# Kernel tuning notes

Measured on AMD Instinct MI355X. Metric: run time of the kernel, lower is better.

## Reference

```python
import jax, jax.numpy as jnp
import numpy as np

B, C, H, W = 4, 512, 128, 128   # batch, in_channels, feature map HxW
KC = 256                        # key_channels
KP = 150                        # number of proxy regions (ADE20K classes)


def conv1x1(x, w, b):
    # x: [b,c,h,w], w: [k,c], b: [k] -> [b,k,h,w]
    return jnp.einsum('bchw,kc->bkhw', x, w) + b[None, :, None, None]


def proj2(x, w1, b1, w2, b2):
    # conv1x1-(BN folded)-relu twice, as in f_pixel / f_object
    h = jax.nn.relu(conv1x1(x, w1, b1))
    return jax.nn.relu(conv1x1(h, w2, b2))


def setup_inputs() -> dict:
    key = jax.random.key(0)
    ks = jax.random.split(key, 16)
    nrm = lambda k, shape, s=0.05: (jax.random.normal(k, shape, jnp.float32) * s)
    return {
        'x': jax.random.normal(ks[0], (B, C, H, W), jnp.float32),
        'proxy_feats': jax.random.normal(ks[1], (B, C, KP, 1), jnp.float32),
        # f_pixel: two 1x1 convs (BN in eval mode folded into weight+bias)
        'w_p1': nrm(ks[2], (KC, C)), 'b_p1': nrm(ks[3], (KC,)),
        'w_p2': nrm(ks[4], (KC, KC)), 'b_p2': nrm(ks[5], (KC,)),
        # f_object
        'w_o1': nrm(ks[6], (KC, C)), 'b_o1': nrm(ks[7], (KC,)),
        'w_o2': nrm(ks[8], (KC, KC)), 'b_o2': nrm(ks[9], (KC,)),
        # f_down
        'w_d': nrm(ks[10], (KC, C)), 'b_d': nrm(ks[11], (KC,)),
        # f_up
        'w_u': nrm(ks[12], (C, KC)), 'b_u': nrm(ks[13], (C,)),
    }


def reference(x, proxy_feats, w_p1, b_p1, w_p2, b_p2, w_o1, b_o1, w_o2, b_o2,
              w_d, b_d, w_u, b_u):
    b, _, h, w = x.shape
    n = h * w
    # query: [b, n, kc]
    query = proj2(x, w_p1, b_p1, w_p2, b_p2).reshape(b, KC, n).transpose(0, 2, 1)
    # key: [b, kc, kp]
    k = proj2(proxy_feats, w_o1, b_o1, w_o2, b_o2).reshape(b, KC, KP)
    # value: [b, kp, kc]
    v = jax.nn.relu(conv1x1(proxy_feats, w_d, b_d)).reshape(b, KC, KP).transpose(0, 2, 1)
    # scaled dot-product cross-attention
    sim = jnp.einsum('bnc,bck->bnk', query, k) * (KC ** -0.5)
    sim = jax.nn.softmax(sim, axis=-1)
    context = jnp.einsum('bnk,bkc->bnc', sim, v)            # [b, n, kc]
    context = context.transpose(0, 2, 1).reshape(b, KC, h, w)
    return jax.nn.relu(conv1x1(context, w_u, b_u))           # [b, C, h, w]
```

## Files before the change

### kernel.cpp

```cpp
#include <hip/hip_runtime.h>
#include <hip/hip_bf16.h>

#define NB   4
#define CIN  512
#define NPX  16384
#define KC   256
#define KP   150

#define LDH  264
#define LDP  200
#define LDX  72
#define SHSZ 16896
#define XBOF 7680

typedef __attribute__((ext_vector_type(8))) short short8;
typedef __attribute__((ext_vector_type(4))) float f32x4;
typedef __attribute__((ext_vector_type(4))) unsigned int u32x4;
typedef unsigned short u16;

__device__ __forceinline__ u16 f2bf(float f) {
    unsigned int u = __float_as_uint(f);
    return (u16)((u + 0x7FFFu + ((u >> 16) & 1u)) >> 16);
}
__device__ __forceinline__ unsigned cvtpk(float lo, float hi) {
    unsigned r;
    asm("v_cvt_pk_bf16_f32 %0, %1, %2" : "=v"(r) : "v"(lo), "v"(hi));
    return r;
}
__device__ __forceinline__ short8 ldfrag(const u16* __restrict__ p, int idx) {
    return *(const short8*)(p + ((long)idx << 3));
}

__global__ __launch_bounds__(256, 4)
void fused_kernel(const u16* __restrict__ wp1p, const float* __restrict__ xg,
                  const u16* __restrict__ wp2p, const float* __restrict__ bp1,
                  const float* __restrict__ bp2, const u16* __restrict__ keyp,
                  const u16* __restrict__ vp, const u16* __restrict__ wup,
                  const float* __restrict__ bu, float* __restrict__ outg)
{
    __shared__ u16 sh[SHSZ];

    const int b  = blockIdx.z;
    const int n0 = blockIdx.x * 64;
    const int tid = threadIdx.x, lane = tid & 63, wid = tid >> 6;
    const int rg = lane & 15, kg = lane >> 4;

    const float* xb = xg + (long)b * CIN * NPX;
    float* ob       = outg + (long)b * CIN * NPX;
    const u16* kyp  = keyp + (long)b * 40960;
    const u16* vbp  = vp   + (long)b * 40960;

    const int sxp = (tid & 31) * 2, sxg = tid >> 5;
    const float* xsrc = xb + (long)(sxg * 8) * NPX + n0 + sxp;
    u16* XB = sh + XBOF;

    float f0[8], f1[8];
    auto LOADX = [&](int kt) {
        #pragma unroll
        for (int e = 0; e < 8; ++e) {
            float2 v = *(const float2*)(xsrc + (long)(kt * 64 + e) * NPX);
            f0[e] = v.x; f1[e] = v.y;
        }
    };
    auto WRITEX = [&](int buf) {
        u32x4 w0, w1;
        w0.x = cvtpk(f0[0], f0[1]); w0.y = cvtpk(f0[2], f0[3]);
        w0.z = cvtpk(f0[4], f0[5]); w0.w = cvtpk(f0[6], f0[7]);
        w1.x = cvtpk(f1[0], f1[1]); w1.y = cvtpk(f1[2], f1[3]);
        w1.z = cvtpk(f1[4], f1[5]); w1.w = cvtpk(f1[6], f1[7]);
        *(u32x4*)(XB + buf * 4608 + sxp * LDX + sxg * 8) = w0;
        *(u32x4*)(XB + buf * 4608 + (sxp + 1) * LDX + sxg * 8) = w1;
    };

    f32x4 acc[4][4];
    #pragma unroll
    for (int i = 0; i < 4; ++i)
        #pragma unroll
        for (int j = 0; j < 4; ++j) acc[i][j] = (f32x4){0.f, 0.f, 0.f, 0.f};

    LOADX(0); WRITEX(0);
    __syncthreads();

    #pragma unroll 1
    for (int kt = 0; kt < 8; ++kt) {
        const int buf = kt & 1;
        if (kt < 7) LOADX(kt + 1);
        #pragma unroll 1
        for (int s = 0; s < 2; ++s) {
            short8 a[4];
            #pragma unroll
            for (int i = 0; i < 4; ++i)
                a[i] = ldfrag(wp1p, ((wid * 4 + i) * 16 + kt * 2 + s) * 64 + lane);
            __builtin_amdgcn_s_setprio(1);
            #pragma unroll
            for (int j = 0; j < 4; ++j) {
                short8 bb = *(const short8*)(XB + buf * 4608 + (j * 16 + rg) * LDX + (s * 4 + kg) * 8);
                #pragma unroll
                for (int i = 0; i < 4; ++i)
                    acc[i][j] = __builtin_amdgcn_mfma_f32_16x16x32_bf16(a[i], bb, acc[i][j], 0, 0, 0);
            }
            __builtin_amdgcn_s_setprio(0);
        }
        if (kt < 7) WRITEX(buf ^ 1);
        __syncthreads();
    }

    #pragma unroll
    for (int i = 0; i < 4; ++i) {
        const int kc4 = wid * 64 + i * 16 + kg * 4;
        const f32x4 bv = *(const f32x4*)(bp1 + kc4);
        #pragma unroll
        for (int j = 0; j < 4; ++j) {
            const int n = j * 16 + rg;
            uint2 pk;
            pk.x = cvtpk(fmaxf(acc[i][j][0] + bv.x, 0.f), fmaxf(acc[i][j][1] + bv.y, 0.f));
            pk.y = cvtpk(fmaxf(acc[i][j][2] + bv.z, 0.f), fmaxf(acc[i][j][3] + bv.w, 0.f));
            *(uint2*)(sh + n * LDH + kc4) = pk;
        }
    }
    __syncthreads();

    f32x4 acc2[4][4];
    #pragma unroll
    for (int i = 0; i < 4; ++i)
        #pragma unroll
        for (int j = 0; j < 4; ++j) acc2[i][j] = (f32x4){0.f, 0.f, 0.f, 0.f};

    #pragma unroll 1
    for (int S = 0; S < 8; ++S) {
        short8 a[4];
        #pragma unroll
        for (int i = 0; i < 4; ++i)
            a[i] = ldfrag(wp2p, ((wid * 4 + i) * 8 + S) * 64 + lane);
        __builtin_amdgcn_s_setprio(1);
        #pragma unroll
        for (int j = 0; j < 4; ++j) {
            short8 bb = *(const short8*)(sh + (j * 16 + rg) * LDH + S * 32 + kg * 8);
            #pragma unroll
            for (int i = 0; i < 4; ++i)
                acc2[i][j] = __builtin_amdgcn_mfma_f32_16x16x32_bf16(a[i], bb, acc2[i][j], 0, 0, 0);
        }
        __builtin_amdgcn_s_setprio(0);
    }
    __syncthreads();

    #pragma unroll
    for (int i = 0; i < 4; ++i) {
        const int kc4 = wid * 64 + i * 16 + kg * 4;
        const f32x4 bv = *(const f32x4*)(bp2 + kc4);
        #pragma unroll
        for (int j = 0; j < 4; ++j) {
            const int n = j * 16 + rg;
            uint2 pk;
            pk.x = cvtpk(fmaxf(acc2[i][j][0] + bv.x, 0.f), fmaxf(acc2[i][j][1] + bv.y, 0.f));
            pk.y = cvtpk(fmaxf(acc2[i][j][2] + bv.z, 0.f), fmaxf(acc2[i][j][3] + bv.w, 0.f));
            *(uint2*)(sh + n * LDH + kc4) = pk;
        }
    }
    __syncthreads();

    f32x4 s1[10];
    #pragma unroll
    for (int i = 0; i < 10; ++i) s1[i] = (f32x4){0.f, 0.f, 0.f, 0.f};
    #pragma unroll 1
    for (int s = 0; s < 8; ++s) {
        short8 bq = *(const short8*)(sh + (wid * 16 + rg) * LDH + s * 32 + kg * 8);
        __builtin_amdgcn_s_setprio(1);
        #pragma unroll
        for (int i = 0; i < 10; ++i) {
            short8 a = ldfrag(kyp, (i * 8 + s) * 64 + lane);
            s1[i] = __builtin_amdgcn_mfma_f32_16x16x32_bf16(a, bq, s1[i], 0, 0, 0);
        }
        __builtin_amdgcn_s_setprio(0);
    }
    float mx = -3.0e38f;
    #pragma unroll
    for (int i = 0; i < 9; ++i)
        #pragma unroll
        for (int r = 0; r < 4; ++r) mx = fmaxf(mx, s1[i][r]);
    #pragma unroll
    for (int r = 0; r < 4; ++r) if (kg * 4 + r < 6) mx = fmaxf(mx, s1[9][r]);
    mx = fmaxf(mx, __shfl_xor(mx, 16));
    mx = fmaxf(mx, __shfl_xor(mx, 32));
    float l = 0.f;
    #pragma unroll
    for (int i = 0; i < 10; ++i)
        #pragma unroll
        for (int r = 0; r < 4; ++r) {
            const bool valid = (i < 9) || (kg * 4 + r < 6);
            float e = valid ? __expf((s1[i][r] - mx) * 0.0625f) : 0.f;
            s1[i][r] = e; l += e;
        }
    l += __shfl_xor(l, 16);
    l += __shfl_xor(l, 32);
    const float inv = 1.f / l;
    __syncthreads();

    #pragma unroll
    for (int i = 0; i < 10; ++i) {
        uint2 pk;
        pk.x = cvtpk(s1[i][0] * inv, s1[i][1] * inv);
        pk.y = cvtpk(s1[i][2] * inv, s1[i][3] * inv);
        *(uint2*)(sh + (wid * 16 + rg) * LDP + i * 16 + kg * 4) = pk;
    }
    __syncthreads();

    f32x4 acc4[4][4];
    #pragma unroll
    for (int i = 0; i < 4; ++i)
        #pragma unroll
        for (int j = 0; j < 4; ++j) acc4[i][j] = (f32x4){0.f, 0.f, 0.f, 0.f};
    #pragma unroll 1
    for (int s = 0; s < 5; ++s) {
        short8 a[4];
        #pragma unroll
        for (int i = 0; i < 4; ++i)
            a[i] = ldfrag(vbp, ((wid * 4 + i) * 5 + s) * 64 + lane);
        __builtin_amdgcn_s_setprio(1);
        #pragma unroll
        for (int j = 0; j < 4; ++j) {
            short8 bb = *(const short8*)(sh + (j * 16 + rg) * LDP + s * 32 + kg * 8);
            #pragma unroll
            for (int i = 0; i < 4; ++i)
                acc4[i][j] = __builtin_amdgcn_mfma_f32_16x16x32_bf16(a[i], bb, acc4[i][j], 0, 0, 0);
        }
        __builtin_amdgcn_s_setprio(0);
    }
    __syncthreads();

    #pragma unroll
    for (int i = 0; i < 4; ++i) {
        const int kc4 = wid * 64 + i * 16 + kg * 4;
        #pragma unroll
        for (int j = 0; j < 4; ++j) {
            const int n = j * 16 + rg;
            uint2 pk;
            pk.x = cvtpk(acc4[i][j][0], acc4[i][j][1]);
            pk.y = cvtpk(acc4[i][j][2], acc4[i][j][3]);
            *(uint2*)(sh + n * LDH + kc4) = pk;
        }
    }
    __syncthreads();

    #pragma unroll 1
    for (int h2 = 0; h2 < 2; ++h2) {
        f32x4 a5[4][4];
        #pragma unroll
        for (int i = 0; i < 4; ++i)
            #pragma unroll
            for (int j = 0; j < 4; ++j) a5[i][j] = (f32x4){0.f, 0.f, 0.f, 0.f};
        #pragma unroll 1
        for (int S = 0; S < 8; ++S) {
            short8 a[4];
            #pragma unroll
            for (int i = 0; i < 4; ++i)
                a[i] = ldfrag(wup, ((h2 * 16 + wid * 4 + i) * 8 + S) * 64 + lane);
            __builtin_amdgcn_s_setprio(1);
            #pragma unroll
            for (int j = 0; j < 4; ++j) {
                short8 bb = *(const short8*)(sh + (j * 16 + rg) * LDH + S * 32 + kg * 8);
                #pragma unroll
                for (int i = 0; i < 4; ++i)
                    a5[i][j] = __builtin_amdgcn_mfma_f32_16x16x32_bf16(a[i], bb, a5[i][j], 0, 0, 0);
            }
            __builtin_amdgcn_s_setprio(0);
        }
        #pragma unroll
        for (int i = 0; i < 4; ++i) {
            const int c4 = h2 * 256 + wid * 64 + i * 16 + kg * 4;
            const f32x4 bv = *(const f32x4*)(bu + c4);
            #pragma unroll
            for (int j = 0; j < 4; ++j) {
                const int n = n0 + j * 16 + rg;
                ob[(long)(c4 + 0) * NPX + n] = fmaxf(a5[i][j][0] + bv.x, 0.f);
                ob[(long)(c4 + 1) * NPX + n] = fmaxf(a5[i][j][1] + bv.y, 0.f);
                ob[(long)(c4 + 2) * NPX + n] = fmaxf(a5[i][j][2] + bv.z, 0.f);
                ob[(long)(c4 + 3) * NPX + n] = fmaxf(a5[i][j][3] + bv.w, 0.f);
            }
        }
    }
}

__global__ __launch_bounds__(256)
void prep_kernel(const float* __restrict__ w_p1, const float* __restrict__ w_p2,
                 const float* __restrict__ w_u,  const float* __restrict__ w_o1,
                 const float* __restrict__ w_o2, const float* __restrict__ w_d,
                 u16* __restrict__ wp1p, u16* __restrict__ wp2p,
                 u16* __restrict__ wup, float* __restrict__ wo1T,
                 float* __restrict__ wdT, float* __restrict__ wo2T)
{
    const int i = blockIdx.x * 256 + threadIdx.x;
    const int j = i & 7, l = (i >> 3) & 63;
    {
        const int S = (i >> 9) & 15, R = i >> 13;
        wp1p[i] = f2bf(w_p1[(long)(R * 16 + (l & 15)) * CIN + S * 32 + ((l >> 4) << 3) + j]);
    }
    {
        const int S = (i >> 9) & 7, R = i >> 12;
        wup[i] = f2bf(w_u[(long)(R * 16 + (l & 15)) * KC + S * 32 + ((l >> 4) << 3) + j]);
    }
    {
        const int c = i >> 8, kc = i & 255;
        wo1T[i] = w_o1[(long)kc * CIN + c];
        wdT[i]  = w_d [(long)kc * CIN + c];
    }
    if (i < 65536) {
        const int S = (i >> 9) & 7, R = i >> 12;
        wp2p[i] = f2bf(w_p2[(long)(R * 16 + (l & 15)) * KC + S * 32 + ((l >> 4) << 3) + j]);
        const int c = i >> 8, kc = i & 255;
        wo2T[i] = w_o2[(long)kc * KC + c];
    }
}

__global__ __launch_bounds__(256)
void kv_kernel(const float* __restrict__ proxy,
               const float* __restrict__ wo1T, const float* __restrict__ b_o1,
               const float* __restrict__ wdT,  const float* __restrict__ b_d,
               const float* __restrict__ wo2T, const float* __restrict__ b_o2,
               u16* __restrict__ keyp, u16* __restrict__ vp)
{
    __shared__ float PX[CIN * 4];
    __shared__ float HL[4][KC];
    const int kp0 = blockIdx.x * 4;
    const int b   = blockIdx.y;
    const int kc  = threadIdx.x;

    #pragma unroll
    for (int it = 0; it < 8; ++it) {
        const int idx = it * 256 + kc;
        const int q = idx & 3, c = idx >> 2;
        const int kp = kp0 + q;
        PX[c * 4 + q] = (kp < KP) ? proxy[(long)b * CIN * KP + (long)c * KP + kp] : 0.f;
    }
    __syncthreads();

    float ah[4] = {0.f, 0.f, 0.f, 0.f}, av[4] = {0.f, 0.f, 0.f, 0.f};
    #pragma unroll 1
    for (int c0 = 0; c0 < CIN; c0 += 8) {
        float w1[8], wd[8];
        #pragma unroll
        for (int e = 0; e < 8; ++e) {
            w1[e] = wo1T[(long)(c0 + e) * KC + kc];
            wd[e] = wdT [(long)(c0 + e) * KC + kc];
        }
        #pragma unroll
        for (int e = 0; e < 8; ++e)
            #pragma unroll
            for (int q = 0; q < 4; ++q) {
                const float p = PX[(c0 + e) * 4 + q];
                ah[q] += w1[e] * p;
                av[q] += wd[e] * p;
            }
    }
    const float bo1 = b_o1[kc], bd = b_d[kc];
    #pragma unroll
    for (int q = 0; q < 4; ++q) {
        const int kp = kp0 + q;
        HL[q][kc] = fmaxf(ah[q] + bo1, 0.f);
        const float vv = (kp < KP) ? fmaxf(av[q] + bd, 0.f) : 0.f;
        const int idx2 = (((kc >> 4) * 5 + (kp >> 5)) * 64 +
                          ((kp >> 3) & 3) * 16 + (kc & 15)) * 8 + (kp & 7);
        vp[(long)b * 40960 + idx2] = f2bf(vv);
    }
    __syncthreads();

    float ak[4] = {0.f, 0.f, 0.f, 0.f};
    #pragma unroll 1
    for (int c0 = 0; c0 < KC; c0 += 8) {
        float w2[8];
        #pragma unroll
        for (int e = 0; e < 8; ++e)
            w2[e] = wo2T[(long)(c0 + e) * KC + kc];
        #pragma unroll
        for (int e = 0; e < 8; ++e)
            #pragma unroll
            for (int q = 0; q < 4; ++q)
                ak[q] += w2[e] * HL[q][c0 + e];
    }
    const float bo2 = b_o2[kc];
    #pragma unroll
    for (int q = 0; q < 4; ++q) {
        const int kp = kp0 + q;
        const float v = (kp < KP) ? fmaxf(ak[q] + bo2, 0.f) : 0.f;
        const int idx = (((kp >> 4) * 8 + (kc >> 5)) * 64 +
                         ((kc >> 3) & 3) * 16 + (kp & 15)) * 8 + (kc & 7);
        keyp[(long)b * 40960 + idx] = f2bf(v);
    }
}

extern "C" void kernel_launch(void* const* d_in, const int* in_sizes, int n_in,
                              void* d_out, int out_size, void* d_ws, size_t ws_size,
                              hipStream_t stream)
{
    const float* x     = (const float*)d_in[0];
    const float* proxy = (const float*)d_in[1];
    const float* w_p1  = (const float*)d_in[2];
    const float* b_p1  = (const float*)d_in[3];
    const float* w_p2  = (const float*)d_in[4];
    const float* b_p2  = (const float*)d_in[5];
    const float* w_o1  = (const float*)d_in[6];
    const float* b_o1  = (const float*)d_in[7];
    const float* w_o2  = (const float*)d_in[8];
    const float* b_o2  = (const float*)d_in[9];
    const float* w_d   = (const float*)d_in[10];
    const float* b_d   = (const float*)d_in[11];
    const float* w_u   = (const float*)d_in[12];
    const float* b_u   = (const float*)d_in[13];
    float* out = (float*)d_out;
    (void)in_sizes; (void)n_in; (void)out_size; (void)ws_size;

    char* ws = (char*)d_ws;
    size_t off = 0;
    auto alloc = [&](size_t bytes) { size_t o = off; off += (bytes + 255) & ~(size_t)255; return o; };

    u16*   wp1p = (u16*)  (ws + alloc((size_t)131072 * 2));
    u16*   wp2p = (u16*)  (ws + alloc((size_t)65536 * 2));
    u16*   wup  = (u16*)  (ws + alloc((size_t)131072 * 2));
    float* wo1T = (float*)(ws + alloc((size_t)131072 * 4));
    float* wdT  = (float*)(ws + alloc((size_t)131072 * 4));
    float* wo2T = (float*)(ws + alloc((size_t)65536 * 4));
    u16*   keyp = (u16*)  (ws + alloc((size_t)NB * 40960 * 2));
    u16*   vp   = (u16*)  (ws + alloc((size_t)NB * 40960 * 2));

    prep_kernel<<<512, 256, 0, stream>>>(
        w_p1, w_p2, w_u, w_o1, w_o2, w_d, wp1p, wp2p, wup, wo1T, wdT, wo2T);
    kv_kernel<<<dim3(40, NB), 256, 0, stream>>>(
        proxy, wo1T, b_o1, wdT, b_d, wo2T, b_o2, keyp, vp);
    fused_kernel<<<dim3(NPX / 64, 1, NB), 256, 0, stream>>>(
        wp1p, x, wp2p, b_p1, b_p2, keyp, vp, wup, b_u, out);
}
```

Measured before the change: 130.2 us.

## Pad X tile stride, tile weight transposes via LDS, split kv kernel finer

Three separate changes. The LDS stride for the bf16 X tile in the fused kernel grows from 72 to 76 elements, and the buffer offset moves, to cut bank conflicts on fragment reads. The weight transposes in prep_kernel now go through 64x64 shared-memory tiles so both global reads and writes are coalesced, handled by extra blocks. kv_kernel processes 2 proxies per block instead of 4, doubling the grid for more parallelism at the cost of reloading the weights twice as often.

```diff
diff --git a/kernel.cpp b/kernel.cpp
--- a/kernel.cpp
+++ b/kernel.cpp
@@ -9,9 +9,9 @@
 
 #define LDH  264
 #define LDP  200
-#define LDX  72
+#define LDX  76
 #define SHSZ 16896
-#define XBOF 7680
+#define XBOF 7168
 
 typedef __attribute__((ext_vector_type(8))) short short8;
 typedef __attribute__((ext_vector_type(4))) float f32x4;
@@ -68,8 +68,8 @@
         w0.z = cvtpk(f0[4], f0[5]); w0.w = cvtpk(f0[6], f0[7]);
         w1.x = cvtpk(f1[0], f1[1]); w1.y = cvtpk(f1[2], f1[3]);
         w1.z = cvtpk(f1[4], f1[5]); w1.w = cvtpk(f1[6], f1[7]);
-        *(u32x4*)(XB + buf * 4608 + sxp * LDX + sxg * 8) = w0;
-        *(u32x4*)(XB + buf * 4608 + (sxp + 1) * LDX + sxg * 8) = w1;
+        *(u32x4*)(XB + buf * 4864 + sxp * LDX + sxg * 8) = w0;
+        *(u32x4*)(XB + buf * 4864 + (sxp + 1) * LDX + sxg * 8) = w1;
     };
 
     f32x4 acc[4][4];
@@ -94,7 +94,7 @@
             __builtin_amdgcn_s_setprio(1);
             #pragma unroll
             for (int j = 0; j < 4; ++j) {
-                short8 bb = *(const short8*)(XB + buf * 4608 + (j * 16 + rg) * LDX + (s * 4 + kg) * 8);
+                short8 bb = *(const short8*)(XB + buf * 4864 + (j * 16 + rg) * LDX + (s * 4 + kg) * 8);
                 #pragma unroll
                 for (int i = 0; i < 4; ++i)
                     acc[i][j] = __builtin_amdgcn_mfma_f32_16x16x32_bf16(a[i], bb, acc[i][j], 0, 0, 0);
@@ -289,27 +289,40 @@
                  u16* __restrict__ wup, float* __restrict__ wo1T,
                  float* __restrict__ wdT, float* __restrict__ wo2T)
 {
-    const int i = blockIdx.x * 256 + threadIdx.x;
-    const int j = i & 7, l = (i >> 3) & 63;
-    {
-        const int S = (i >> 9) & 15, R = i >> 13;
-        wp1p[i] = f2bf(w_p1[(long)(R * 16 + (l & 15)) * CIN + S * 32 + ((l >> 4) << 3) + j]);
-    }
-    {
-        const int S = (i >> 9) & 7, R = i >> 12;
-        wup[i] = f2bf(w_u[(long)(R * 16 + (l & 15)) * KC + S * 32 + ((l >> 4) << 3) + j]);
-    }
-    {
-        const int c = i >> 8, kc = i & 255;
-        wo1T[i] = w_o1[(long)kc * CIN + c];
-        wdT[i]  = w_d [(long)kc * CIN + c];
-    }
-    if (i < 65536) {
-        const int S = (i >> 9) & 7, R = i >> 12;
-        wp2p[i] = f2bf(w_p2[(long)(R * 16 + (l & 15)) * KC + S * 32 + ((l >> 4) << 3) + j]);
-        const int c = i >> 8, kc = i & 255;
-        wo2T[i] = w_o2[(long)kc * KC + c];
-    }
+    const int bx = blockIdx.x;
+    const int tid = threadIdx.x;
+    if (bx < 512) {
+        const int i = bx * 256 + tid;
+        const int j = i & 7, l = (i >> 3) & 63;
+        {
+            const int S = (i >> 9) & 15, R = i >> 13;
+            wp1p[i] = f2bf(w_p1[(long)(R * 16 + (l & 15)) * CIN + S * 32 + ((l >> 4) << 3) + j]);
+        }
+        {
+            const int S = (i >> 9) & 7, R = i >> 12;
+            wup[i] = f2bf(w_u[(long)(R * 16 + (l & 15)) * KC + S * 32 + ((l >> 4) << 3) + j]);
+        }
+        if (i < 65536) {
+            const int S = (i >> 9) & 7, R = i >> 12;
+            wp2p[i] = f2bf(w_p2[(long)(R * 16 + (l & 15)) * KC + S * 32 + ((l >> 4) << 3) + j]);
+        }
+        return;
+    }
+    __shared__ float T[64][65];
+    int tb = bx - 512;
+    const float* src; float* dst; int srcC;
+    if (tb < 32)      { src = w_o1; dst = wo1T; srcC = CIN; }
+    else if (tb < 64) { tb -= 32; src = w_d; dst = wdT; srcC = CIN; }
+    else              { tb -= 64; src = w_o2; dst = wo2T; srcC = KC; }
+    const int r0 = (tb & 3) * 64, c0 = (tb >> 2) * 64;
+    const int lr = tid >> 6, lc = tid & 63;
+    #pragma unroll
+    for (int p = 0; p < 16; ++p)
+        T[p * 4 + lr][lc] = src[(long)(r0 + p * 4 + lr) * srcC + c0 + lc];
+    __syncthreads();
+    #pragma unroll
+    for (int p = 0; p < 16; ++p)
+        dst[(long)(c0 + p * 4 + lr) * KC + r0 + lc] = T[lc][p * 4 + lr];
 }
 
 __global__ __launch_bounds__(256)
@@ -319,22 +332,22 @@
                const float* __restrict__ wo2T, const float* __restrict__ b_o2,
                u16* __restrict__ keyp, u16* __restrict__ vp)
 {
-    __shared__ float PX[CIN * 4];
-    __shared__ float HL[4][KC];
-    const int kp0 = blockIdx.x * 4;
+    __shared__ float PX[CIN * 2];
+    __shared__ float HL[2][KC];
+    const int kp0 = blockIdx.x * 2;
     const int b   = blockIdx.y;
     const int kc  = threadIdx.x;
 
     #pragma unroll
-    for (int it = 0; it < 8; ++it) {
+    for (int it = 0; it < 4; ++it) {
         const int idx = it * 256 + kc;
-        const int q = idx & 3, c = idx >> 2;
+        const int q = idx & 1, c = idx >> 1;
         const int kp = kp0 + q;
-        PX[c * 4 + q] = (kp < KP) ? proxy[(long)b * CIN * KP + (long)c * KP + kp] : 0.f;
-    }
-    __syncthreads();
-
-    float ah[4] = {0.f, 0.f, 0.f, 0.f}, av[4] = {0.f, 0.f, 0.f, 0.f};
+        PX[c * 2 + q] = (kp < KP) ? proxy[(long)b * CIN * KP + (long)c * KP + kp] : 0.f;
+    }
+    __syncthreads();
+
+    float ah[2] = {0.f, 0.f}, av[2] = {0.f, 0.f};
     #pragma unroll 1
     for (int c0 = 0; c0 < CIN; c0 += 8) {
         float w1[8], wd[8];
@@ -346,15 +359,15 @@
         #pragma unroll
         for (int e = 0; e < 8; ++e)
             #pragma unroll
-            for (int q = 0; q < 4; ++q) {
-                const float p = PX[(c0 + e) * 4 + q];
+            for (int q = 0; q < 2; ++q) {
+                const float p = PX[(c0 + e) * 2 + q];
                 ah[q] += w1[e] * p;
                 av[q] += wd[e] * p;
             }
     }
     const float bo1 = b_o1[kc], bd = b_d[kc];
     #pragma unroll
-    for (int q = 0; q < 4; ++q) {
+    for (int q = 0; q < 2; ++q) {
         const int kp = kp0 + q;
         HL[q][kc] = fmaxf(ah[q] + bo1, 0.f);
         const float vv = (kp < KP) ? fmaxf(av[q] + bd, 0.f) : 0.f;
@@ -364,7 +377,7 @@
     }
     __syncthreads();
 
-    float ak[4] = {0.f, 0.f, 0.f, 0.f};
+    float ak[2] = {0.f, 0.f};
     #pragma unroll 1
     for (int c0 = 0; c0 < KC; c0 += 8) {
         float w2[8];
@@ -374,12 +387,12 @@
         #pragma unroll
         for (int e = 0; e < 8; ++e)
             #pragma unroll
-            for (int q = 0; q < 4; ++q)
+            for (int q = 0; q < 2; ++q)
                 ak[q] += w2[e] * HL[q][c0 + e];
     }
     const float bo2 = b_o2[kc];
     #pragma unroll
-    for (int q = 0; q < 4; ++q) {
+    for (int q = 0; q < 2; ++q) {
         const int kp = kp0 + q;
         const float v = (kp < KP) ? fmaxf(ak[q] + bo2, 0.f) : 0.f;
         const int idx = (((kp >> 4) * 8 + (kc >> 5)) * 64 +
@@ -422,9 +435,9 @@
     u16*   keyp = (u16*)  (ws + alloc((size_t)NB * 40960 * 2));
     u16*   vp   = (u16*)  (ws + alloc((size_t)NB * 40960 * 2));
 
-    prep_kernel<<<512, 256, 0, stream>>>(
+    prep_kernel<<<592, 256, 0, stream>>>(
         w_p1, w_p2, w_u, w_o1, w_o2, w_d, wp1p, wp2p, wup, wo1T, wdT, wo2T);
-    kv_kernel<<<dim3(40, NB), 256, 0, stream>>>(
+    kv_kernel<<<dim3(80, NB), 256, 0, stream>>>(
         proxy, wo1T, b_o1, wdT, b_d, wo2T, b_o2, keyp, vp);
     fused_kernel<<<dim3(NPX / 64, 1, NB), 256, 0, stream>>>(
         wp1p, x, wp2p, b_p1, b_p2, keyp, vp, wup, b_u, out);
```

Measured after the change: 130.1 us (median of 2 runs). No clear change (-0.0%).
